# Kernel optimization log

Measured on AMD Instinct MI355X. Metric: run time of the kernel, lower is better.

## Reference

```python
import jax, jax.numpy as jnp
import numpy as np


def _binarize(w):
    # sign(w) with sign(0) mapped to +1, matching the torch forward
    return jnp.where(w >= 0, 1.0, -1.0).astype(w.dtype)


def setup_inputs() -> dict:
    key = jax.random.key(0)
    k1, k2, k3 = jax.random.split(key, 3)
    N, IN, OUT = 8192, 4096, 4096
    x = jax.random.normal(k1, (N, IN), dtype=jnp.float32)
    weight = jax.random.normal(k2, (OUT, IN), dtype=jnp.float32)
    fan_in = IN
    bound = 1.0 / fan_in ** 0.5
    bias = jax.random.uniform(k3, (OUT,), dtype=jnp.float32, minval=-bound, maxval=bound)
    return {"x": x, "weight": weight, "bias": bias}


def reference(x, weight, bias):
    # forward: clamp(-1,1) then sign-binarize; clamp does not change the sign,
    # so binarized weight is simply sign(weight) with 0 -> +1.
    w_clamped = jnp.clip(weight, -1.0, 1.0)
    bw = _binarize(w_clamped)  # [OUT, IN] of +/-1
    # F.linear: x @ W^T + b
    return jnp.einsum('ni,oi->no', x, bw) + bias
```

## Files before the change

kernel.cpp:

```cpp
#include <hip/hip_runtime.h>
#include <stdint.h>

#define M_DIM 8192
#define N_DIM 4096
#define K_DIM 4096

typedef __attribute__((ext_vector_type(4))) int int32x4;

#define QUANT_BLOCKS 2048
#define SIGN_BLOCKS  1024
#define SIGN_THREADS (SIGN_BLOCKS * 256)

__global__ __launch_bounds__(256) void prep_kernel(const float* __restrict__ x,
                                                   const float* __restrict__ w,
                                                   signed char* __restrict__ xq,
                                                   signed char* __restrict__ wq,
                                                   float* __restrict__ scales) {
  const int bid = blockIdx.x;
  const int t = threadIdx.x;
  if (bid < QUANT_BLOCKS) {
    const int wave = t >> 6, lane = t & 63;
    const int row = bid * 4 + wave;
    const float4* xr = (const float4*)(x + (size_t)row * K_DIM);
    float4 v[16];
    float amax = 0.f;
#pragma unroll
    for (int j = 0; j < 16; j++) {
      v[j] = xr[lane + 64 * j];
      amax = fmaxf(amax, fmaxf(fmaxf(fabsf(v[j].x), fabsf(v[j].y)),
                               fmaxf(fabsf(v[j].z), fabsf(v[j].w))));
    }
#pragma unroll
    for (int off = 32; off > 0; off >>= 1)
      amax = fmaxf(amax, __shfl_xor(amax, off, 64));
    amax = fmaxf(amax, 1e-30f);
    const float rsc = 127.0f / amax;
    if (lane == 0) scales[row] = amax / 127.0f;
    int* qr = (int*)(xq + (size_t)row * K_DIM);
#pragma unroll
    for (int j = 0; j < 16; j++) {
      int q0 = __float2int_rn(v[j].x * rsc);
      int q1 = __float2int_rn(v[j].y * rsc);
      int q2 = __float2int_rn(v[j].z * rsc);
      int q3 = __float2int_rn(v[j].w * rsc);
      qr[lane + 64 * j] = (q0 & 255) | ((q1 & 255) << 8) | ((q2 & 255) << 16) | (q3 << 24);
    }
  } else {
    const int idx0 = (bid - QUANT_BLOCKS) * 256 + t;
    const float4* wf = (const float4*)w;
    int4* o = (int4*)wq;
#pragma unroll
    for (int k = 0; k < 4; k++) {
      const int idx = idx0 + k * SIGN_THREADS;
      int4 pk;
      int* pi = (int*)&pk;
#pragma unroll
      for (int j = 0; j < 4; j++) {
        float4 a = wf[(size_t)idx * 4 + j];
        unsigned b0 = a.x >= 0.f ? 0x01u : 0xFFu;
        unsigned b1 = a.y >= 0.f ? 0x01u : 0xFFu;
        unsigned b2 = a.z >= 0.f ? 0x01u : 0xFFu;
        unsigned b3 = a.w >= 0.f ? 0x01u : 0xFFu;
        pi[j] = (int)(b0 | (b1 << 8) | (b2 << 16) | (b3 << 24));
      }
      o[idx] = pk;
    }
  }
}

__device__ __forceinline__ void async16(const signed char* g, signed char* l) {
  __builtin_amdgcn_global_load_lds((const __attribute__((address_space(1))) void*)g,
                                   (__attribute__((address_space(3))) void*)l, 16, 0, 0);
}

__global__ __launch_bounds__(256) void gemm_i8_kernel(
    const signed char* __restrict__ A,
    const signed char* __restrict__ B,
    const float* __restrict__ scales,
    const float* __restrict__ bias,
    float* __restrict__ C) {
  __shared__ signed char la[128 * 128];
  __shared__ signed char lb[128 * 128];

  const int tid  = threadIdx.x;
  const int wave = tid >> 6;
  const int lane = tid & 63;
  const int wm = wave >> 1, wn = wave & 1;
  const int qd = lane >> 4, l16 = lane & 15;
  const long m0 = (long)blockIdx.y * 128;
  const long n0 = (long)blockIdx.x * 128;

  const signed char* gA[4];
  const signed char* gB[4];
  signed char* lA[4];
  signed char* lB[4];
#pragma unroll
  for (int q = 0; q < 4; q++) {
    const int c = q * 256 + wave * 64 + lane;
    const int r = c >> 3, s = c & 7;
    const int off = (s ^ (r & 7)) * 16;
    gA[q] = A + (m0 + r) * K_DIM + off;
    gB[q] = B + (n0 + r) * K_DIM + off;
    lA[q] = &la[(q * 256 + wave * 64) * 16];
    lB[q] = &lb[(q * 256 + wave * 64) * 16];
  }

  const int swz = l16 & 7;
  const int32x4* pa[4][2];
  const int32x4* pb[4][2];
#pragma unroll
  for (int t = 0; t < 4; t++) {
#pragma unroll
    for (int kk = 0; kk < 2; kk++) {
      pa[t][kk] = (const int32x4*)&la[(wm * 64 + t * 16 + l16) * 128 + ((kk * 4 + qd) ^ swz) * 16];
      pb[t][kk] = (const int32x4*)&lb[(wn * 64 + t * 16 + l16) * 128 + ((kk * 4 + qd) ^ swz) * 16];
    }
  }

  int32x4 acc[4][4];
#pragma unroll
  for (int i = 0; i < 4; i++)
#pragma unroll
    for (int j = 0; j < 4; j++)
      acc[i][j] = (int32x4){0, 0, 0, 0};

  for (int k0 = 0; k0 < K_DIM; k0 += 128) {
#pragma unroll
    for (int q = 0; q < 4; q++) {
      async16(gA[q] + k0, lA[q]);
      async16(gB[q] + k0, lB[q]);
    }
    __syncthreads();

#pragma unroll
    for (int kk = 0; kk < 2; kk++) {
      int32x4 af[4], bf[4];
#pragma unroll
      for (int t = 0; t < 4; t++) { af[t] = *pa[t][kk]; bf[t] = *pb[t][kk]; }
#pragma unroll
      for (int i = 0; i < 4; i++)
#pragma unroll
        for (int j = 0; j < 4; j++)
          acc[i][j] = __builtin_amdgcn_mfma_i32_16x16x64_i8(af[i], bf[j], acc[i][j], 0, 0, 0);
    }

    __syncthreads();
  }

  const long row0 = m0 + wm * 64 + qd * 4;
  const long col0 = n0 + wn * 64 + l16;
#pragma unroll
  for (int tj = 0; tj < 4; tj++) {
    float bv = bias[col0 + tj * 16];
#pragma unroll
    for (int ti = 0; ti < 4; ti++) {
      long r = row0 + ti * 16;
      float4 sv = *(const float4*)&scales[r];
      const float* s = &sv.x;
#pragma unroll
      for (int i = 0; i < 4; i++) {
        C[(r + i) * N_DIM + col0 + tj * 16] = (float)acc[ti][tj][i] * s[i] + bv;
      }
    }
  }
}

extern "C" void kernel_launch(void* const* d_in, const int* in_sizes, int n_in,
                              void* d_out, int out_size, void* d_ws, size_t ws_size,
                              hipStream_t stream) {
  const float* x    = (const float*)d_in[0];
  const float* w    = (const float*)d_in[1];
  const float* bias = (const float*)d_in[2];
  float* out = (float*)d_out;

  signed char* xq = (signed char*)d_ws;
  signed char* wq = xq + (size_t)M_DIM * K_DIM;
  float* scales   = (float*)(wq + (size_t)N_DIM * K_DIM);

  prep_kernel<<<QUANT_BLOCKS + SIGN_BLOCKS, 256, 0, stream>>>(x, w, xq, wq, scales);

  dim3 grid(N_DIM / 128, M_DIM / 128);
  gemm_i8_kernel<<<grid, 256, 0, stream>>>(xq, wq, scales, bias, out);
}
```

Before: 402.8 us.

## Rework int8 GEMM into 256x256 tiles with double-buffered async LDS pipeline

Replaces the 128x128 single-buffered int8 GEMM with 256x256 tiles over 512 threads, each wave computing 128x64. Global-to-LDS loads are double-buffered and interleaved with MFMA phases, using explicit barriers, waitcnt and setprio. A workgroup index remap is added for L2 locality. This targets load latency stalls and raises operand reuse, but uses 128KB of LDS and more accumulator registers, which limits occupancy.

```diff
diff --git a/kernel.cpp b/kernel.cpp
--- a/kernel.cpp
+++ b/kernel.cpp
@@ -4,6 +4,7 @@
 #define M_DIM 8192
 #define N_DIM 4096
 #define K_DIM 4096
+#define NT    (K_DIM / 128)
 
 typedef __attribute__((ext_vector_type(4))) int int32x4;
 
@@ -73,93 +74,137 @@
                                    (__attribute__((address_space(3))) void*)l, 16, 0, 0);
 }
 
-__global__ __launch_bounds__(256) void gemm_i8_kernel(
+
+#define STAGE_A(b, h, k0)                                                      \
+  do {                                                                         \
+    async16(gA + (h) * (128L * K_DIM) + (k0),                                  \
+            &lds[(b) * 32768 + (h) * 16384 + wave * 1024]);                    \
+    async16(gA + (h) * (128L * K_DIM) + 64L * K_DIM + (k0),                    \
+            &lds[(b) * 32768 + (h) * 16384 + 8192 + wave * 1024]);             \
+  } while (0)
+
+#define STAGE_B(b, h, k0)                                                      \
+  do {                                                                         \
+    async16(gB + (h) * (128L * K_DIM) + (k0),                                  \
+            &lds[65536 + (b) * 32768 + (h) * 16384 + wave * 1024]);            \
+    async16(gB + (h) * (128L * K_DIM) + 64L * K_DIM + (k0),                    \
+            &lds[65536 + (b) * 32768 + (h) * 16384 + 8192 + wave * 1024]);     \
+  } while (0)
+
+#define PHASE(BUF, Q, STAGE_STMT, TAIL_STMT)                                   \
+  {                                                                            \
+    int32x4 af[2][2];                                                          \
+    _Pragma("unroll") for (int i2 = 0; i2 < 2; ++i2)                           \
+    _Pragma("unroll") for (int kk = 0; kk < 2; ++kk)                           \
+      af[i2][kk] = *(const int32x4*)&lds[(BUF) * 32768 + aoff[kk] +            \
+                                         (2 * (Q) + i2) * 2048];               \
+    STAGE_STMT;                                                                \
+    __builtin_amdgcn_s_barrier();                                              \
+    asm volatile("s_waitcnt lgkmcnt(0)" ::: "memory");                         \
+    __builtin_amdgcn_sched_barrier(0);                                         \
+    __builtin_amdgcn_s_setprio(1);                                             \
+    _Pragma("unroll") for (int kk = 0; kk < 2; ++kk)                           \
+    _Pragma("unroll") for (int i2 = 0; i2 < 2; ++i2)                           \
+    _Pragma("unroll") for (int fj = 0; fj < 4; ++fj)                           \
+      acc[2 * (Q) + i2][fj] = __builtin_amdgcn_mfma_i32_16x16x64_i8(           \
+          af[i2][kk], bfr[fj][kk], acc[2 * (Q) + i2][fj], 0, 0, 0);            \
+    __builtin_amdgcn_s_setprio(0);                                             \
+    TAIL_STMT;                                                                 \
+    __builtin_amdgcn_s_barrier();                                              \
+  }
+
+#define WINDOW(BUF, KA, KB)                                                    \
+  {                                                                            \
+    int32x4 bfr[4][2];                                                         \
+    _Pragma("unroll") for (int fj = 0; fj < 4; ++fj)                           \
+    _Pragma("unroll") for (int kk = 0; kk < 2; ++kk)                           \
+      bfr[fj][kk] =                                                            \
+          *(const int32x4*)&lds[(BUF) * 32768 + boff[kk] + fj * 2048];         \
+    PHASE(BUF, 0, STAGE_A(1 - (BUF), 0, KA), (void)0)                          \
+    PHASE(BUF, 1, STAGE_A(1 - (BUF), 1, KA), (void)0)                          \
+    PHASE(BUF, 2, STAGE_B(BUF, 0, KB), (void)0)                                \
+    PHASE(BUF, 3, STAGE_B(BUF, 1, KB),                                         \
+          asm volatile("s_waitcnt vmcnt(4)" ::: "memory"))                     \
+  }
+
+__global__ __launch_bounds__(512, 2) void gemm_i8_kernel(
     const signed char* __restrict__ A,
     const signed char* __restrict__ B,
     const float* __restrict__ scales,
     const float* __restrict__ bias,
     float* __restrict__ C) {
-  __shared__ signed char la[128 * 128];
-  __shared__ signed char lb[128 * 128];
+  __shared__ __align__(16) signed char lds[131072];
 
   const int tid  = threadIdx.x;
   const int wave = tid >> 6;
   const int lane = tid & 63;
-  const int wm = wave >> 1, wn = wave & 1;
+  const int wm = wave >> 2;
+  const int wn = wave & 3;
   const int qd = lane >> 4, l16 = lane & 15;
-  const long m0 = (long)blockIdx.y * 128;
-  const long n0 = (long)blockIdx.x * 128;
-
-  const signed char* gA[4];
-  const signed char* gB[4];
-  signed char* lA[4];
-  signed char* lB[4];
-#pragma unroll
-  for (int q = 0; q < 4; q++) {
-    const int c = q * 256 + wave * 64 + lane;
-    const int r = c >> 3, s = c & 7;
-    const int off = (s ^ (r & 7)) * 16;
-    gA[q] = A + (m0 + r) * K_DIM + off;
-    gB[q] = B + (n0 + r) * K_DIM + off;
-    lA[q] = &la[(q * 256 + wave * 64) * 16];
-    lB[q] = &lb[(q * 256 + wave * 64) * 16];
-  }
+
+  int wg = blockIdx.x;
+  wg = (wg & 7) * (512 / 8) + (wg >> 3);
+  const int bx = wg & 15;
+  const int by = wg >> 4;
+  const long m0 = (long)by * 256;
+  const long n0 = (long)bx * 256;
+
+  const int roff = tid >> 3;
+  const int poff = ((tid & 7) ^ ((tid >> 3) & 7)) << 4;
+  const signed char* gA = A + (m0 + roff) * K_DIM + poff;
+  const signed char* gB = B + (n0 + roff) * K_DIM + poff;
 
   const int swz = l16 & 7;
-  const int32x4* pa[4][2];
-  const int32x4* pb[4][2];
-#pragma unroll
-  for (int t = 0; t < 4; t++) {
-#pragma unroll
-    for (int kk = 0; kk < 2; kk++) {
-      pa[t][kk] = (const int32x4*)&la[(wm * 64 + t * 16 + l16) * 128 + ((kk * 4 + qd) ^ swz) * 16];
-      pb[t][kk] = (const int32x4*)&lb[(wn * 64 + t * 16 + l16) * 128 + ((kk * 4 + qd) ^ swz) * 16];
-    }
-  }
-
-  int32x4 acc[4][4];
-#pragma unroll
-  for (int i = 0; i < 4; i++)
-#pragma unroll
-    for (int j = 0; j < 4; j++)
+  int aoff[2], boff[2];
+#pragma unroll
+  for (int kk = 0; kk < 2; ++kk) {
+    const int pp = ((kk * 4 + qd) ^ swz) << 4;
+    aoff[kk] = (wm * 128 + l16) * 128 + pp;
+    boff[kk] = 65536 + (wn * 64 + l16) * 128 + pp;
+  }
+
+  int32x4 acc[8][4];
+#pragma unroll
+  for (int i = 0; i < 8; ++i)
+#pragma unroll
+    for (int j = 0; j < 4; ++j)
       acc[i][j] = (int32x4){0, 0, 0, 0};
 
-  for (int k0 = 0; k0 < K_DIM; k0 += 128) {
-#pragma unroll
-    for (int q = 0; q < 4; q++) {
-      async16(gA[q] + k0, lA[q]);
-      async16(gB[q] + k0, lB[q]);
-    }
-    __syncthreads();
-
-#pragma unroll
-    for (int kk = 0; kk < 2; kk++) {
-      int32x4 af[4], bf[4];
-#pragma unroll
-      for (int t = 0; t < 4; t++) { af[t] = *pa[t][kk]; bf[t] = *pb[t][kk]; }
-#pragma unroll
-      for (int i = 0; i < 4; i++)
-#pragma unroll
-        for (int j = 0; j < 4; j++)
-          acc[i][j] = __builtin_amdgcn_mfma_i32_16x16x64_i8(af[i], bf[j], acc[i][j], 0, 0, 0);
-    }
-
-    __syncthreads();
-  }
-
-  const long row0 = m0 + wm * 64 + qd * 4;
+  STAGE_A(0, 0, 0);
+  STAGE_A(0, 1, 0);
+  STAGE_B(0, 0, 0);
+  STAGE_B(0, 1, 0);
+  STAGE_B(1, 0, 128);
+  STAGE_B(1, 1, 128);
+  asm volatile("s_waitcnt vmcnt(4)" ::: "memory");
+  __builtin_amdgcn_s_barrier();
+
+#pragma unroll 1
+  for (int W = 0; W < NT; W += 2) {
+    const long kA0 = (long)((W + 1 < NT) ? (W + 1) : (NT - 1)) * 128;
+    const long kB0 = (long)((W + 2 < NT) ? (W + 2) : (NT - 1)) * 128;
+    WINDOW(0, kA0, kB0)
+    const long kA1 = (long)((W + 2 < NT) ? (W + 2) : (NT - 1)) * 128;
+    const long kB1 = (long)((W + 3 < NT) ? (W + 3) : (NT - 1)) * 128;
+    WINDOW(1, kA1, kB1)
+  }
+
+  asm volatile("s_waitcnt vmcnt(0)" ::: "memory");
+  __builtin_amdgcn_s_barrier();
+
+  const long row0 = m0 + wm * 128 + qd * 4;
   const long col0 = n0 + wn * 64 + l16;
 #pragma unroll
-  for (int tj = 0; tj < 4; tj++) {
-    float bv = bias[col0 + tj * 16];
-#pragma unroll
-    for (int ti = 0; ti < 4; ti++) {
-      long r = row0 + ti * 16;
+  for (int fj = 0; fj < 4; ++fj) {
+    const float bv = bias[col0 + fj * 16];
+#pragma unroll
+    for (int fi = 0; fi < 8; ++fi) {
+      const long r = row0 + fi * 16;
       float4 sv = *(const float4*)&scales[r];
       const float* s = &sv.x;
 #pragma unroll
-      for (int i = 0; i < 4; i++) {
-        C[(r + i) * N_DIM + col0 + tj * 16] = (float)acc[ti][tj][i] * s[i] + bv;
+      for (int i = 0; i < 4; ++i) {
+        C[(r + i) * N_DIM + col0 + fj * 16] = (float)acc[fi][fj][i] * s[i] + bv;
       }
     }
   }
@@ -179,6 +224,6 @@
 
   prep_kernel<<<QUANT_BLOCKS + SIGN_BLOCKS, 256, 0, stream>>>(x, w, xq, wq, scales);
 
-  dim3 grid(N_DIM / 128, M_DIM / 128);
-  gemm_i8_kernel<<<grid, 256, 0, stream>>>(xq, wq, scales, bias, out);
-}
+  gemm_i8_kernel<<<dim3((M_DIM / 256) * (N_DIM / 256)), dim3(512), 0, stream>>>(
+      xq, wq, scales, bias, out);
+}
```

Result: faster. 392.4 us (-2.6%).
